# Optimization experiments

Measured on AMD Instinct MI355X. Metric: run time of the kernel, lower is better.

## Reference

```python
import jax, jax.numpy as jnp
import numpy as np

B, TE, TD, HE, HD = 8, 256, 128, 512, 512


def setup_inputs() -> dict:
    key = jax.random.key(0)
    k1, k2, k3, k4, k5 = jax.random.split(key, 5)
    # scale weights down (original uses 'uniform' init) to keep tanh unsaturated
    return {
        "encoder_out_seq": jax.random.normal(k1, (B, TE, HE), dtype=jnp.float32),
        "decoder_out_seq": jax.random.normal(k2, (B, TD, HD), dtype=jnp.float32),
        "W_a": jax.random.normal(k3, (HE, HE), dtype=jnp.float32) * 0.05,
        "U_a": jax.random.normal(k4, (HD, HE), dtype=jnp.float32) * 0.05,
        "V_a": jax.random.normal(k5, (HE, 1), dtype=jnp.float32) * 0.05,
    }


def reference(encoder_out_seq, decoder_out_seq, W_a, U_a, V_a):
    # Bahdanau additive attention, vectorized over all decoder timesteps
    # (the original loops over Td via K.rnn; steps are independent).
    Ws = jnp.einsum('bte,eh->bth', encoder_out_seq, W_a)   # [B, Te, He]
    Uh = jnp.einsum('bdk,kh->bdh', decoder_out_seq, U_a)   # [B, Td, He]
    # tanh(S.Wa + h.Ua): broadcast to [B, Td, Te, He], contract with V_a
    act = jnp.tanh(Ws[:, None, :, :] + Uh[:, :, None, :])  # [B, Td, Te, He]
    e = jnp.einsum('bdth,ho->bdt', act, V_a)                # [B, Td, Te]
    e = jax.nn.softmax(e, axis=-1)                          # attention weights
    c = jnp.einsum('bdt,bth->bdh', e, encoder_out_seq)      # [B, Td, He] contexts
    return (c, e)
```

## Files before the change

kernel.cpp:

```cpp
#include <hip/hip_runtime.h>

#define B_  8
#define TE_ 256
#define TD_ 128
#define HE_ 512

typedef __attribute__((ext_vector_type(8))) short short8v;
typedef __attribute__((ext_vector_type(4))) float f32x4;

__global__ __launch_bounds__(512) void gemm_fused(
    const float* __restrict__ enc, const float* __restrict__ dec,
    const float* __restrict__ Wa, const float* __restrict__ Ua,
    float* __restrict__ C) {
  __shared__ short BT[2][32][512];
  const int bid = blockIdx.x;
  const int mt = bid % 24, nt = bid / 24;
  const int m0 = mt * 128, n0 = nt * 32;
  const float* Bsrc = (mt < 16) ? Wa : Ua;
  const float* Asrc = (mt < 16) ? enc + (size_t)m0 * 512
                                : dec + (size_t)(m0 - 2048) * 512;
  const int tid = threadIdx.x;
  {
    const int kp = tid >> 3;
    const int c4 = (tid & 7) * 4;
    for (int p = 0; p < 4; ++p) {
      const int k = 2 * kp + p * 128;
      float4 v0 = *(const float4*)(Bsrc + (size_t)k * 512 + n0 + c4);
      float4 v1 = *(const float4*)(Bsrc + (size_t)(k + 1) * 512 + n0 + c4);
      const float a0[4] = {v0.x, v0.y, v0.z, v0.w};
      const float a1[4] = {v1.x, v1.y, v1.z, v1.w};
      const int kc = k >> 3, klo = k & 7;
#pragma unroll
      for (int q = 0; q < 4; ++q) {
        const int n = c4 + q;
        unsigned u0 = __float_as_uint(a0[q]);
        unsigned u1 = __float_as_uint(a1[q]);
        unsigned hi32 = __builtin_amdgcn_perm(u1, u0, 0x07060302);
        float l0 = a0[q] - __uint_as_float(u0 & 0xffff0000u);
        float l1 = a1[q] - __uint_as_float(u1 & 0xffff0000u);
        unsigned lo32 = __builtin_amdgcn_perm(__float_as_uint(l1), __float_as_uint(l0), 0x07060302);
        const int slot = (kc & ~7) | ((kc ^ n) & 7);
        *(unsigned*)&BT[0][n][slot * 8 + klo] = hi32;
        *(unsigned*)&BT[1][n][slot * 8 + klo] = lo32;
      }
    }
  }
  __syncthreads();
  const int w = tid >> 6, lane = tid & 63;
  const int fm = lane & 15, fc = lane >> 4;
  const float* Ap = Asrc + (size_t)(w * 16 + fm) * 512 + fc * 8;
  f32x4 acc0 = {}, acc1 = {};
  float4 pfa[2], pfb[2];
  pfa[0] = *(const float4*)(Ap);
  pfb[0] = *(const float4*)(Ap + 4);
  pfa[1] = *(const float4*)(Ap + 32);
  pfb[1] = *(const float4*)(Ap + 36);
  for (int it = 0; it < 16; ++it) {
    const float4 fa = pfa[it & 1];
    const float4 fb = pfb[it & 1];
    if (it < 14) {
      pfa[it & 1] = *(const float4*)(Ap + (it + 2) * 32);
      pfb[it & 1] = *(const float4*)(Ap + (it + 2) * 32 + 4);
    }
    const float af[8] = {fa.x, fa.y, fa.z, fa.w, fb.x, fb.y, fb.z, fb.w};
    union { unsigned u[4]; short8v s; } ahu, alu;
#pragma unroll
    for (int e = 0; e < 4; ++e) {
      unsigned u0 = __float_as_uint(af[2 * e]);
      unsigned u1 = __float_as_uint(af[2 * e + 1]);
      ahu.u[e] = __builtin_amdgcn_perm(u1, u0, 0x07060302);
      float l0 = af[2 * e]     - __uint_as_float(u0 & 0xffff0000u);
      float l1 = af[2 * e + 1] - __uint_as_float(u1 & 0xffff0000u);
      alu.u[e] = __builtin_amdgcn_perm(__float_as_uint(l1), __float_as_uint(l0), 0x07060302);
    }
    const short8v ah = ahu.s, al = alu.s;
    const int kc = it * 4 + fc;
    const int base = kc & ~7;
    const int s0 = (base | ((kc ^ fm) & 7)) * 8;
    const int s1 = (base | ((kc ^ (16 + fm)) & 7)) * 8;
    short8v bh0 = *(const short8v*)&BT[0][fm][s0];
    short8v bl0 = *(const short8v*)&BT[1][fm][s0];
    short8v bh1 = *(const short8v*)&BT[0][16 + fm][s1];
    short8v bl1 = *(const short8v*)&BT[1][16 + fm][s1];
    acc0 = __builtin_amdgcn_mfma_f32_16x16x32_bf16(ah, bh0, acc0, 0, 0, 0);
    acc1 = __builtin_amdgcn_mfma_f32_16x16x32_bf16(ah, bh1, acc1, 0, 0, 0);
    acc0 = __builtin_amdgcn_mfma_f32_16x16x32_bf16(ah, bl0, acc0, 0, 0, 0);
    acc1 = __builtin_amdgcn_mfma_f32_16x16x32_bf16(ah, bl1, acc1, 0, 0, 0);
    acc0 = __builtin_amdgcn_mfma_f32_16x16x32_bf16(al, bh0, acc0, 0, 0, 0);
    acc1 = __builtin_amdgcn_mfma_f32_16x16x32_bf16(al, bh1, acc1, 0, 0, 0);
  }
  const int row = m0 + w * 16 + fc * 4;
  float* Cp = C + (size_t)row * 512 + n0 + fm;
#pragma unroll
  for (int r = 0; r < 4; ++r) Cp[(size_t)r * 512] = acc0[r];
#pragma unroll
  for (int r = 0; r < 4; ++r) Cp[(size_t)r * 512 + 16] = acc1[r];
}

#define C2 2.8853900817779268f
__global__ __launch_bounds__(1024) void attn_fused(
    const float* __restrict__ Ws, const float* __restrict__ Uh,
    const float* __restrict__ Va, const float* __restrict__ enc,
    float* __restrict__ c_out, float* __restrict__ e_out) {
  __shared__ float sUh[4][HE_];
  __shared__ float sV[HE_];
  __shared__ float sE[4][TE_];
  __shared__ float sRed[16];
  __shared__ float sNorm[4];
  const int tid = threadIdx.x;
  const int b  = blockIdx.x & 7;
  const int d0 = (blockIdx.x >> 3) * 4;
  if (tid < 512)
    ((float4*)sUh)[tid] = ((const float4*)(Uh + (size_t)(b * TD_ + d0) * HE_))[tid];
  else if (tid < 640)
    ((float4*)sV)[tid - 512] = ((const float4*)Va)[tid - 512];
  __syncthreads();
  const int lane = tid & 63, w = tid >> 6;
  const int tb = w * 16;
  const int h0 = lane * 8;
  float eU[4][8], vv2[8], sumv = 0.f;
#pragma unroll
  for (int j = 0; j < 8; ++j) {
    const float vj = sV[h0 + j];
    sumv += vj;
    vv2[j] = 2.0f * vj;
#pragma unroll
    for (int d = 0; d < 4; ++d)
      eU[d][j] = __builtin_amdgcn_exp2f(C2 * sUh[d][h0 + j]);
  }
  const float* pw = Ws + ((size_t)b * TE_ + tb) * HE_ + h0;
  float4 a0 = *(const float4*)(pw);
  float4 a1 = *(const float4*)(pw + 4);
  float s0, s1, s2, s3;
#define TELT4(X, J) { \
    float EW = __builtin_amdgcn_exp2f(C2 * (X)); \
    float E0 = EW * eU[0][J], E1 = EW * eU[1][J]; \
    float E2 = EW * eU[2][J], E3 = EW * eU[3][J]; \
    float r0 = __builtin_amdgcn_rcpf(E0 + 1.0f); \
    float r1 = __builtin_amdgcn_rcpf(E1 + 1.0f); \
    float r2 = __builtin_amdgcn_rcpf(E2 + 1.0f); \
    float r3 = __builtin_amdgcn_rcpf(E3 + 1.0f); \
    s0 = fmaf(-vv2[J], r0, s0); s1 = fmaf(-vv2[J], r1, s1); \
    s2 = fmaf(-vv2[J], r2, s2); s3 = fmaf(-vv2[J], r3, s3); }
  for (int ti = 0; ti < 16; ++ti) {
    const float* pn = pw + HE_;
    float4 n0 = *(const float4*)(pn);
    float4 n1 = *(const float4*)(pn + 4);
    s0 = s1 = s2 = s3 = sumv;
    TELT4(a0.x, 0) TELT4(a0.y, 1) TELT4(a0.z, 2) TELT4(a0.w, 3)
    TELT4(a1.x, 4) TELT4(a1.y, 5) TELT4(a1.z, 6) TELT4(a1.w, 7)
#pragma unroll
    for (int off = 32; off; off >>= 1) {
      s0 += __shfl_down(s0, off, 64);
      s1 += __shfl_down(s1, off, 64);
      s2 += __shfl_down(s2, off, 64);
      s3 += __shfl_down(s3, off, 64);
    }
    if (lane == 0) {
      sE[0][tb + ti] = s0; sE[1][tb + ti] = s1;
      sE[2][tb + ti] = s2; sE[3][tb + ti] = s3;
    }
    a0 = n0; a1 = n1;
    pw = pn;
  }
  __syncthreads();
  const int dA = tid >> 8, t = tid & 255;
  const float ex = __expf(sE[dA][t]);
  float sum = ex;
#pragma unroll
  for (int off = 32; off; off >>= 1) sum += __shfl_down(sum, off, 64);
  if (lane == 0) sRed[w] = sum;
  __syncthreads();
  if (tid < 4)
    sNorm[tid] = 1.0f / (sRed[tid * 4] + sRed[tid * 4 + 1] + sRed[tid * 4 + 2] + sRed[tid * 4 + 3]);
  __syncthreads();
  const float wgt = ex * sNorm[dA];
  sE[dA][t] = wgt;
  e_out[(size_t)(b * TD_ + d0 + dA) * TE_ + t] = wgt;
  __syncthreads();
  const int h = tid & 511;
  const int db = (tid >> 9) * 2;
  float a0c = 0.f, a1c = 0.f;
  const float* ep = enc + (size_t)b * TE_ * HE_ + h;
  const float* e0 = sE[db];
  const float* e1 = sE[db + 1];
#pragma unroll 4
  for (int tt = 0; tt < TE_; ++tt) {
    const float ev = ep[(size_t)tt * HE_];
    a0c = fmaf(e0[tt], ev, a0c);
    a1c = fmaf(e1[tt], ev, a1c);
  }
  float* cp = c_out + (size_t)(b * TD_ + d0 + db) * HE_ + h;
  cp[0]   = a0c;
  cp[HE_] = a1c;
}

extern "C" void kernel_launch(void* const* d_in, const int* in_sizes, int n_in,
                              void* d_out, int out_size, void* d_ws, size_t ws_size,
                              hipStream_t stream) {
  const float* enc = (const float*)d_in[0];
  const float* dec = (const float*)d_in[1];
  const float* Wa  = (const float*)d_in[2];
  const float* Ua  = (const float*)d_in[3];
  const float* Va  = (const float*)d_in[4];
  float* c_out = (float*)d_out;
  float* e_out = c_out + (size_t)B_ * TD_ * HE_;
  float* Cws = (float*)d_ws;
  const float* Ws = Cws;
  const float* Uh = Cws + (size_t)2048 * 512;
  gemm_fused<<<384, 512, 0, stream>>>(enc, dec, Wa, Ua, Cws);
  attn_fused<<<256, 1024, 0, stream>>>(Ws, Uh, Va, enc, c_out, e_out);
}
```

Baseline: 126.5 us.

## Halve decoder rows per attention block and use DPP wave reductions

Result: faster. 121.8 us (-3.7%).

```diff
diff --git a/kernel.cpp b/kernel.cpp
--- a/kernel.cpp
+++ b/kernel.cpp
@@ -7,6 +7,19 @@
 
 typedef __attribute__((ext_vector_type(8))) short short8v;
 typedef __attribute__((ext_vector_type(4))) float f32x4;
+
+__device__ __forceinline__ float wave_red_add(float s) {
+#define DPPADD(CTRL) \
+  s += __int_as_float(__builtin_amdgcn_update_dpp(0, __float_as_int(s), CTRL, 0xf, 0xf, true))
+  DPPADD(0x111);
+  DPPADD(0x112);
+  DPPADD(0x114);
+  DPPADD(0x118);
+  DPPADD(0x142);
+  DPPADD(0x143);
+#undef DPPADD
+  return s;
+}
 
 __global__ __launch_bounds__(512) void gemm_fused(
     const float* __restrict__ enc, const float* __restrict__ dec,
@@ -102,97 +115,84 @@
     const float* __restrict__ Ws, const float* __restrict__ Uh,
     const float* __restrict__ Va, const float* __restrict__ enc,
     float* __restrict__ c_out, float* __restrict__ e_out) {
-  __shared__ float sUh[4][HE_];
+  __shared__ float sUh[2][HE_];
   __shared__ float sV[HE_];
-  __shared__ float sE[4][TE_];
-  __shared__ float sRed[16];
-  __shared__ float sNorm[4];
+  __shared__ float sE[2][TE_];
+  __shared__ float sRed[8];
+  __shared__ float sNorm[2];
   const int tid = threadIdx.x;
   const int b  = blockIdx.x & 7;
-  const int d0 = (blockIdx.x >> 3) * 4;
-  if (tid < 512)
+  const int d0 = (blockIdx.x >> 3) * 2;
+  if (tid < 256)
     ((float4*)sUh)[tid] = ((const float4*)(Uh + (size_t)(b * TD_ + d0) * HE_))[tid];
-  else if (tid < 640)
-    ((float4*)sV)[tid - 512] = ((const float4*)Va)[tid - 512];
+  else if (tid < 384)
+    ((float4*)sV)[tid - 256] = ((const float4*)Va)[tid - 256];
   __syncthreads();
   const int lane = tid & 63, w = tid >> 6;
   const int tb = w * 16;
   const int h0 = lane * 8;
-  float eU[4][8], vv2[8], sumv = 0.f;
+  float eU[2][8], vv2[8], sumv = 0.f;
 #pragma unroll
   for (int j = 0; j < 8; ++j) {
     const float vj = sV[h0 + j];
     sumv += vj;
     vv2[j] = 2.0f * vj;
-#pragma unroll
-    for (int d = 0; d < 4; ++d)
-      eU[d][j] = __builtin_amdgcn_exp2f(C2 * sUh[d][h0 + j]);
+    eU[0][j] = __builtin_amdgcn_exp2f(C2 * sUh[0][h0 + j]);
+    eU[1][j] = __builtin_amdgcn_exp2f(C2 * sUh[1][h0 + j]);
   }
   const float* pw = Ws + ((size_t)b * TE_ + tb) * HE_ + h0;
   float4 a0 = *(const float4*)(pw);
   float4 a1 = *(const float4*)(pw + 4);
-  float s0, s1, s2, s3;
-#define TELT4(X, J) { \
+  float s0, s1;
+#define TELT2(X, J) { \
     float EW = __builtin_amdgcn_exp2f(C2 * (X)); \
     float E0 = EW * eU[0][J], E1 = EW * eU[1][J]; \
-    float E2 = EW * eU[2][J], E3 = EW * eU[3][J]; \
     float r0 = __builtin_amdgcn_rcpf(E0 + 1.0f); \
     float r1 = __builtin_amdgcn_rcpf(E1 + 1.0f); \
-    float r2 = __builtin_amdgcn_rcpf(E2 + 1.0f); \
-    float r3 = __builtin_amdgcn_rcpf(E3 + 1.0f); \
-    s0 = fmaf(-vv2[J], r0, s0); s1 = fmaf(-vv2[J], r1, s1); \
-    s2 = fmaf(-vv2[J], r2, s2); s3 = fmaf(-vv2[J], r3, s3); }
+    s0 = fmaf(-vv2[J], r0, s0); s1 = fmaf(-vv2[J], r1, s1); }
   for (int ti = 0; ti < 16; ++ti) {
     const float* pn = pw + HE_;
     float4 n0 = *(const float4*)(pn);
     float4 n1 = *(const float4*)(pn + 4);
-    s0 = s1 = s2 = s3 = sumv;
-    TELT4(a0.x, 0) TELT4(a0.y, 1) TELT4(a0.z, 2) TELT4(a0.w, 3)
-    TELT4(a1.x, 4) TELT4(a1.y, 5) TELT4(a1.z, 6) TELT4(a1.w, 7)
-#pragma unroll
-    for (int off = 32; off; off >>= 1) {
-      s0 += __shfl_down(s0, off, 64);
-      s1 += __shfl_down(s1, off, 64);
-      s2 += __shfl_down(s2, off, 64);
-      s3 += __shfl_down(s3, off, 64);
-    }
-    if (lane == 0) {
-      sE[0][tb + ti] = s0; sE[1][tb + ti] = s1;
-      sE[2][tb + ti] = s2; sE[3][tb + ti] = s3;
+    s0 = s1 = sumv;
+    TELT2(a0.x, 0) TELT2(a0.y, 1) TELT2(a0.z, 2) TELT2(a0.w, 3)
+    TELT2(a1.x, 4) TELT2(a1.y, 5) TELT2(a1.z, 6) TELT2(a1.w, 7)
+    s0 = wave_red_add(s0);
+    s1 = wave_red_add(s1);
+    if (lane == 63) {
+      sE[0][tb + ti] = s0;
+      sE[1][tb + ti] = s1;
     }
     a0 = n0; a1 = n1;
     pw = pn;
   }
   __syncthreads();
-  const int dA = tid >> 8, t = tid & 255;
-  const float ex = __expf(sE[dA][t]);
-  float sum = ex;
-#pragma unroll
-  for (int off = 32; off; off >>= 1) sum += __shfl_down(sum, off, 64);
-  if (lane == 0) sRed[w] = sum;
-  __syncthreads();
-  if (tid < 4)
-    sNorm[tid] = 1.0f / (sRed[tid * 4] + sRed[tid * 4 + 1] + sRed[tid * 4 + 2] + sRed[tid * 4 + 3]);
-  __syncthreads();
-  const float wgt = ex * sNorm[dA];
-  sE[dA][t] = wgt;
-  e_out[(size_t)(b * TD_ + d0 + dA) * TE_ + t] = wgt;
+  if (tid < 512) {
+    const int dA = tid >> 8, t = tid & 255;
+    const float ex = __expf(sE[dA][t]);
+    float sum = wave_red_add(ex);
+    if (lane == 63) sRed[w] = sum;
+    __syncthreads();
+    if (tid < 2)
+      sNorm[tid] = 1.0f / (sRed[tid * 4] + sRed[tid * 4 + 1] + sRed[tid * 4 + 2] + sRed[tid * 4 + 3]);
+    __syncthreads();
+    const float wgt = ex * sNorm[dA];
+    sE[dA][t] = wgt;
+    e_out[(size_t)(b * TD_ + d0 + dA) * TE_ + t] = wgt;
+  } else {
+    __syncthreads();
+    __syncthreads();
+  }
   __syncthreads();
   const int h = tid & 511;
-  const int db = (tid >> 9) * 2;
-  float a0c = 0.f, a1c = 0.f;
+  const int dd = tid >> 9;
+  float acc = 0.f;
   const float* ep = enc + (size_t)b * TE_ * HE_ + h;
-  const float* e0 = sE[db];
-  const float* e1 = sE[db + 1];
-#pragma unroll 4
-  for (int tt = 0; tt < TE_; ++tt) {
-    const float ev = ep[(size_t)tt * HE_];
-    a0c = fmaf(e0[tt], ev, a0c);
-    a1c = fmaf(e1[tt], ev, a1c);
-  }
-  float* cp = c_out + (size_t)(b * TD_ + d0 + db) * HE_ + h;
-  cp[0]   = a0c;
-  cp[HE_] = a1c;
+  const float* ew = sE[dd];
+#pragma unroll 8
+  for (int tt = 0; tt < TE_; ++tt)
+    acc = fmaf(ew[tt], ep[(size_t)tt * HE_], acc);
+  c_out[(size_t)(b * TD_ + d0 + dd) * HE_ + h] = acc;
 }
 
 extern "C" void kernel_launch(void* const* d_in, const int* in_sizes, int n_in,
@@ -209,5 +209,5 @@
   const float* Ws = Cws;
   const float* Uh = Cws + (size_t)2048 * 512;
   gemm_fused<<<384, 512, 0, stream>>>(enc, dec, Wa, Ua, Cws);
-  attn_fused<<<256, 1024, 0, stream>>>(Ws, Uh, Va, enc, c_out, e_out);
-}
+  attn_fused<<<512, 1024, 0, stream>>>(Ws, Uh, Va, enc, c_out, e_out);
+}
```
